# Kernel tuning notes

Hardware: AMD Instinct MI355X
Metric: run time of the kernel (lower is better)

## Reference

```python
import jax, jax.numpy as jnp
import numpy as np

# Dimensions
B, T = 128, 512
H = 256            # lstm_hiddens; encoder width is 2*H
LIN = 200          # linear_hiddens (LSTMCell input size)
PD, WD = 50, 20    # pos_dims, wordlen_dims
PN, WN = 32, 8     # pos_num, wordlen_num (word len clipped to 7)
SP = 58            # segpos_num
APP_ID = 0         # id of the APP action (forbidden at t=0)


def setup_inputs() -> dict:
    key = jax.random.key(0)
    ks = jax.random.split(key, 13)
    enc = jax.random.normal(ks[0], (B, T, 2 * H), dtype=jnp.float32)
    sep_mask = jax.random.randint(ks[1], (B, T), 0, 2, dtype=jnp.int32)
    sep_mask = sep_mask.at[:, 0].set(1)  # first action is always SEP (APP forbidden at t=0)
    pos_ids = jax.random.randint(ks[2], (B, T), 0, PN, dtype=jnp.int32)
    length = jax.random.randint(ks[3], (B,), T // 2, T + 1, dtype=jnp.int32)
    s = 0.05
    pos_emb = jax.random.normal(ks[4], (PN, PD), dtype=jnp.float32) * s
    wordlen_emb = jax.random.normal(ks[5], (WN, WD), dtype=jnp.float32) * s
    fc_W = jax.random.normal(ks[6], (LIN, PD + 2 * H + WD), dtype=jnp.float32) * s
    fc_b = jax.random.normal(ks[7], (LIN,), dtype=jnp.float32) * s
    W_ih = jax.random.normal(ks[8], (4 * H, LIN), dtype=jnp.float32) * s
    W_hh = jax.random.normal(ks[9], (4 * H, H), dtype=jnp.float32) * s
    b_ih = jax.random.normal(ks[10], (4 * H,), dtype=jnp.float32) * s
    b_hh = jax.random.normal(ks[11], (4 * H,), dtype=jnp.float32) * s
    combine_W = jax.random.normal(ks[12], (SP, 3 * H), dtype=jnp.float32) * s
    return {"encoder_output": enc, "sep_mask": sep_mask, "pos_ids": pos_ids,
            "length": length, "pos_emb": pos_emb, "wordlen_emb": wordlen_emb,
            "fc_W": fc_W, "fc_b": fc_b, "W_ih": W_ih, "W_hh": W_hh,
            "b_ih": b_ih, "b_hh": b_hh, "combine_W": combine_W}


def reference(encoder_output, sep_mask, pos_ids, length, pos_emb, wordlen_emb,
              fc_W, fc_b, W_ih, W_hh, b_ih, b_hh, combine_W):
    b, t, h2 = encoder_output.shape
    h = h2 // 2
    idx = jnp.arange(t, dtype=jnp.int32)

    # last SEP position strictly before t (word start of the in-progress word)
    sep_pos = jnp.where(sep_mask > 0, idx[None, :], 0)            # [B,T]
    cmax = jax.lax.cummax(sep_pos, axis=1)                        # last sep <= t
    last_sep = jnp.concatenate(
        [jnp.zeros((b, 1), jnp.int32), cmax[:, :-1]], axis=1)     # last sep < t

    wlen = idx[None, :] - last_sep                                # [B,T]; >=1 for t>=1
    wlen_safe = jnp.maximum(wlen, 1)
    wlen_id = jnp.minimum(wlen_safe, 7)                           # clip: len>6 -> 7

    # mean of encoder states over the current word [last_sep, t) via cumsum
    csum = jnp.concatenate(
        [jnp.zeros((b, 1, h2), encoder_output.dtype),
         jnp.cumsum(encoder_output, axis=1)], axis=1)             # [B,T+1,2H]
    start_sum = jnp.take_along_axis(csum, last_sep[:, :, None], axis=1)
    word_avg = (csum[:, :t] - start_sum) / wlen_safe[:, :, None].astype(encoder_output.dtype)

    last_pos = jnp.take_along_axis(pos_ids, last_sep, axis=1)     # [B,T]
    feats = jnp.concatenate(
        [pos_emb[last_pos], word_avg, wordlen_emb[wlen_id]], axis=-1)  # [B,T,PD+2H+WD]
    z = jnp.tanh(jnp.einsum('btf,lf->btl', feats, fc_W) + fc_b)   # [B,T,LIN]
    z = z.at[:, 0].set(0.0)                                       # step 0 input is zeros

    # LSTMCell recurrence over time (torch gate order: i, f, g, o)
    def step(carry, zt):
        hh, cc = carry
        g = zt @ W_ih.T + b_ih + hh @ W_hh.T + b_hh               # [B,4H]
        i, f, gg, o = jnp.split(g, 4, axis=-1)
        cc = jax.nn.sigmoid(f) * cc + jax.nn.sigmoid(i) * jnp.tanh(gg)
        hh = jax.nn.sigmoid(o) * jnp.tanh(cc)
        return (hh, cc), hh

    h0 = jnp.zeros((b, h), encoder_output.dtype)
    _, hs = jax.lax.scan(step, (h0, h0), jnp.swapaxes(z, 0, 1))   # hs: [T,B,H]
    hs = jnp.swapaxes(hs, 0, 1)                                   # [B,T,H]

    v = jnp.concatenate([hs, encoder_output], axis=-1)            # [B,T,3H]
    logits = jnp.einsum('btv,sv->bts', v, combine_W)              # [B,T,SP]
    logits = logits.at[:, 0, APP_ID].set(-1e30)                   # forbid APP at t=0 (in-place, no grad)
    valid = (idx[None, :] < length[:, None])[:, :, None]
    logits = jnp.where(valid, logits, 0.0)                        # pad steps emit zeros
    return logits.reshape(b * t, SP)
```

## Files before the change

### kernel.cpp

```cpp
#include <hip/hip_runtime.h>

typedef unsigned short ushort_t;
typedef unsigned int uint32;
typedef __attribute__((ext_vector_type(8))) short short8;
typedef __attribute__((ext_vector_type(4))) short short4v;
typedef __attribute__((ext_vector_type(4))) float floatx4;
typedef __attribute__((ext_vector_type(2))) float float2v;
typedef __attribute__((ext_vector_type(8))) int intx8;

#define B_    128
#define T_    512
#define H_    256
#define H2_   512
#define LIN_  200
#define LINP_ 224
#define G4_   1024
#define SP_   58
#define BT_   (B_*T_)

#define OFF_LS     0UL
#define OFF_LP     262144UL
#define OFF_WID    524288UL
#define OFF_INV    786432UL
#define OFF_POSW   1212416UL
#define OFF_WLW    1238016UL
#define OFF_BIASG  1244416UL
#define OFF_WHH    1248512UL
#define OFF_WIH    1772800UL
#define OFF_WENC   2231552UL
#define OFF_COMBW  2436352UL
#define OFF_ECW    2525440UL
#define OFF_Z      28739840UL
#define OFF_GPERM  58099968UL
#define OFF_VBF    192317696UL

__device__ __forceinline__ ushort_t f2bf(float x){
  uint32 u = __float_as_uint(x);
  u += 0x7fffu + ((u >> 16) & 1u);
  return (ushort_t)(u >> 16);
}
__device__ __forceinline__ float bf2f(ushort_t v){
  return __uint_as_float(((uint32)v) << 16);
}
__device__ __forceinline__ float fsig(float x){
  return __builtin_amdgcn_rcpf(1.0f + __expf(-x));
}
__device__ __forceinline__ float ftanh(float x){
  return 1.0f - 2.0f * __builtin_amdgcn_rcpf(1.0f + __expf(2.0f * x));
}

__global__ __launch_bounds__(512) void k_scan(const int* __restrict__ sep, const int* __restrict__ pos_ids,
                       int* __restrict__ ls, int* __restrict__ lp,
                       int* __restrict__ wid, float* __restrict__ inv){
  int b = blockIdx.x, t = threadIdx.x;
  __shared__ int sm[512];
  int v = (sep[b*T_ + t] > 0) ? t : 0;
  sm[t] = v;
  __syncthreads();
  #pragma unroll
  for (int off = 1; off < 512; off <<= 1){
    int o = (t >= off) ? sm[t - off] : 0;
    __syncthreads();
    v = (o > v) ? o : v;
    sm[t] = v;
    __syncthreads();
  }
  int l = (t == 0) ? 0 : sm[t - 1];
  int wlen = t - l;
  int wsv  = (wlen < 1) ? 1 : wlen;
  ls[b*T_ + t]  = l;
  lp[b*T_ + t]  = pos_ids[b*T_ + l];
  wid[b*T_ + t] = (wsv > 7) ? 7 : wsv;
  inv[b*T_ + t] = 1.0f / (float)wsv;
}

__global__ __launch_bounds__(256) void k_encbf(const float* __restrict__ enc, ushort_t* __restrict__ vbf){
  const long total = (long)BT_ * 128;
  for (long i = (long)blockIdx.x * 256 + threadIdx.x; i < total; i += 2048L * 256){
    floatx4 v = ((const floatx4*)enc)[i];
    long row = i >> 7;
    int c4 = (int)(i & 127);
    int b = (int)(row >> 9), t = (int)(row & (T_-1));
    short4v pk;
    pk[0] = (short)f2bf(v[0]); pk[1] = (short)f2bf(v[1]);
    pk[2] = (short)f2bf(v[2]); pk[3] = (short)f2bf(v[3]);
    *(short4v*)(void*)(vbf + ((long)t * B_ + b) * 768 + 256 + c4*4) = pk;
  }
}

__global__ __launch_bounds__(256) void k_small(
    const float* __restrict__ pos_emb, const float* __restrict__ wl_emb,
    const float* __restrict__ fcW, const float* __restrict__ W_ih,
    const float* __restrict__ W_hh, const float* __restrict__ b_ih,
    const float* __restrict__ b_hh, const float* __restrict__ combW,
    float* __restrict__ posW, float* __restrict__ wlW, float* __restrict__ biasg,
    char* __restrict__ whh8, ushort_t* __restrict__ wih,
    ushort_t* __restrict__ wenc, ushort_t* __restrict__ combwb){
  int idx = blockIdx.x * 256 + threadIdx.x;
  if (idx < 6400){
    int p = idx / 200, l = idx % 200;
    float s = 0.f;
    for (int d = 0; d < 50; d++) s += pos_emb[p*50 + d] * fcW[l*582 + d];
    posW[idx] = s; return;
  }
  idx -= 6400;
  if (idx < 1600){
    int w = idx / 200, l = idx % 200;
    float s = 0.f;
    for (int d = 0; d < 20; d++) s += wl_emb[w*20 + d] * fcW[l*582 + 562 + d];
    wlW[idx] = s; return;
  }
  idx -= 1600;
  if (idx < 1024){ biasg[idx] = b_ih[idx] + b_hh[idx]; return; }
  idx -= 1024;
  if (idx < 262144){
    int p8 = __builtin_amdgcn_cvt_pk_fp8_f32(W_hh[idx], W_hh[idx], 0, false);
    whh8[idx] = (char)(p8 & 0xff);
    return;
  }
  idx -= 262144;
  if (idx < 229376){
    int n = idx / 224, k = idx % 224;
    wih[idx] = (k < 200) ? f2bf(W_ih[n*200 + k]) : (ushort_t)0;
    return;
  }
  idx -= 229376;
  if (idx < 102400){
    int l = idx / 512, c = idx % 512;
    wenc[idx] = f2bf(fcW[l*582 + 50 + c]); return;
  }
  idx -= 102400;
  if (idx < 44544){ combwb[idx] = f2bf(combW[idx]); return; }
}

template<int EPI>
__global__ __launch_bounds__(256) void k_gemm(
    const ushort_t* __restrict__ A, long lda,
    const ushort_t* __restrict__ Bm, int K, int Nvalid,
    void* __restrict__ Cout, const float* __restrict__ bias, const int* __restrict__ len){
  __shared__ __attribute__((aligned(16))) ushort_t As[64][48];
  __shared__ __attribute__((aligned(16))) ushort_t Bs[64][48];
  int tid  = threadIdx.x;
  int lane = tid & 63, wave = tid >> 6;
  int u = lane & 15, quad = lane >> 4;
  int mh = wave >> 1, nh = wave & 1;
  long m0 = (long)blockIdx.y * 64;
  int  n0 = blockIdx.x * 64;
  int lrow = tid >> 2;
  int lcol = (tid & 3) * 8;
  const ushort_t* Arow = A + (m0 + lrow) * lda + lcol;
  bool bvalid = (n0 + lrow) < Nvalid;
  const ushort_t* Brow = Bm + (long)(n0 + lrow) * K + lcol;
  floatx4 acc[2][2] = {};
  for (int k = 0; k < K; k += 32){
    short8 av = *(const short8*)(const void*)(Arow + k);
    short8 bv = {0,0,0,0,0,0,0,0};
    if (bvalid) bv = *(const short8*)(const void*)(Brow + k);
    __syncthreads();
    *(short8*)(void*)&As[lrow][lcol] = av;
    *(short8*)(void*)&Bs[lrow][lcol] = bv;
    __syncthreads();
    short8 a0 = *(const short8*)(const void*)&As[mh*32 + u][quad*8];
    short8 a1 = *(const short8*)(const void*)&As[mh*32 + 16 + u][quad*8];
    short8 b0 = *(const short8*)(const void*)&Bs[nh*32 + u][quad*8];
    short8 b1 = *(const short8*)(const void*)&Bs[nh*32 + 16 + u][quad*8];
    acc[0][0] = __builtin_amdgcn_mfma_f32_16x16x32_bf16(a0, b0, acc[0][0], 0, 0, 0);
    acc[0][1] = __builtin_amdgcn_mfma_f32_16x16x32_bf16(a0, b1, acc[0][1], 0, 0, 0);
    acc[1][0] = __builtin_amdgcn_mfma_f32_16x16x32_bf16(a1, b0, acc[1][0], 0, 0, 0);
    acc[1][1] = __builtin_amdgcn_mfma_f32_16x16x32_bf16(a1, b1, acc[1][1], 0, 0, 0);
  }
  if (EPI == 1){
    #pragma unroll
    for (int mi = 0; mi < 2; mi++){
      #pragma unroll
      for (int ni = 0; ni < 2; ni++){
        long mm = m0 + mh*32 + mi*16 + quad*4;
        int n = n0 + nh*32 + ni*16 + u;
        float bv = bias[n];
        int t = (int)(mm >> 7);
        int b = (int)(mm & 127);
        int blk = b >> 2;
        int g = n >> 8, j = n & 255, ut = j & 15, jt = j >> 4;
        long idx = ((((long)t*32 + blk)*16 + jt)*4 + g)*64 + ut*4;
        short4v pk;
        #pragma unroll
        for (int r = 0; r < 4; r++) pk[r] = (short)f2bf(acc[mi][ni][r] + bv);
        *(short4v*)(void*)((ushort_t*)Cout + idx) = pk;
      }
    }
  } else {
    for (int mi = 0; mi < 2; mi++){
      for (int ni = 0; ni < 2; ni++){
        for (int r = 0; r < 4; r++){
          long m = m0 + mh*32 + mi*16 + quad*4 + r;
          int  n = n0 + nh*32 + ni*16 + u;
          float v = acc[mi][ni][r];
          if (EPI == 0){
            if (n < Nvalid) ((ushort_t*)Cout)[m * Nvalid + n] = f2bf(v);
          } else {
            if (n < Nvalid){
              int t = (int)(m >> 7); int b = (int)(m & 127);
              float o = (t < len[b]) ? v : 0.0f;
              if (t == 0 && n == 0) o = -1e30f;
              ((float*)Cout)[((long)b * T_ + t) * SP_ + n] = o;
            }
          }
        }
      }
    }
  }
}

__global__ __launch_bounds__(256) void k_cum200(ushort_t* __restrict__ E){
  int b = blockIdx.x;
  int c = threadIdx.x;
  if (c >= LIN_) return;
  float acc = 0.f;
  ushort_t* p = E + (long)b * LIN_ + c;
  const long rs = (long)B_ * LIN_;
  for (int t0 = 0; t0 < T_; t0 += 16){
    float vv[16];
    #pragma unroll
    for (int i = 0; i < 16; i++) vv[i] = bf2f(p[i*rs]);
    #pragma unroll
    for (int i = 0; i < 16; i++){ p[i*rs] = f2bf(acc); acc += vv[i]; }
    p += 16*rs;
  }
}

__global__ __launch_bounds__(256) void k_z(
    const ushort_t* __restrict__ CW, const int* __restrict__ ls, const int* __restrict__ lp,
    const int* __restrict__ wid, const float* __restrict__ inv,
    const float* __restrict__ posW, const float* __restrict__ wlW,
    const float* __restrict__ fcb, ushort_t* __restrict__ zbf){
  int l = threadIdx.x;
  if (l >= LINP_) return;
  float fb = (l < LIN_) ? fcb[l] : 0.f;
  #pragma unroll
  for (int i = 0; i < 8; i++){
    int m = blockIdx.x * 8 + i;
    int t = m >> 7;
    int b = m & 127;
    int ar = b * T_ + t;
    ushort_t o = 0;
    if (t != 0 && l < LIN_){
      int lsv = ls[ar];
      float x = bf2f(CW[(long)m * LIN_ + l]) - bf2f(CW[((long)lsv * B_ + b) * LIN_ + l]);
      x = x * inv[ar] + posW[lp[ar]*LIN_ + l] + wlW[wid[ar]*LIN_ + l] + fb;
      o = f2bf(ftanh(x));
    }
    zbf[(long)m * LINP_ + l] = o;
  }
}

__global__ __launch_bounds__(1024, 4) void k_rec(
    const ushort_t* __restrict__ Gperm, const char* __restrict__ whh8,
    ushort_t* __restrict__ vbf){
  int blk  = blockIdx.x;
  int tid  = threadIdx.x;
  int lane = tid & 63, w = tid >> 6;
  int u = lane & 15, quad = lane >> 4;
  __shared__ __attribute__((aligned(16))) char h8[2][16][272];
  for (int i = tid; i < (int)(sizeof(h8)/4); i += 1024) ((int*)h8)[i] = 0;

  intx8 wfx[4][2];
  #pragma unroll
  for (int g = 0; g < 4; g++){
    int grow = g*256 + w*16 + u;
    #pragma unroll
    for (int kc = 0; kc < 2; kc++){
      intx8 v = *(const intx8*)(const void*)(whh8 + (long)grow*256 + kc*128 + quad*32);
      asm volatile("" : "+v"(v));
      wfx[g][kc] = v;
    }
  }
  float c_reg = 0.f;
  floatx4 acc[4] = {};

  const ushort_t* gp0 = Gperm + ((long)blk*16 + w)*256 + (long)u*4 + quad;
  ushort_t gb[4];
  #pragma unroll
  for (int g = 0; g < 4; g++) gb[g] = gp0[g*64];

  for (int t = 0; t < T_; t++){
    #pragma unroll
    for (int g = 0; g < 4; g++) acc[g][0] = bf2f(gb[g]);
    asm volatile("s_waitcnt lgkmcnt(0)\n\ts_barrier" ::: "memory");
    intx8 af0 = *(const intx8*)(const void*)&h8[t & 1][u][quad*32];
    intx8 af1 = *(const intx8*)(const void*)&h8[t & 1][u][128 + quad*32];
    if (t && w < 4){
      ushort_t* vrow = vbf + ((long)(t-1) * B_ + blk*4 + w) * 768;
      uint32 p = *(const uint32*)(const void*)&h8[t & 1][4*w][lane*4];
      float2v lo = __builtin_amdgcn_cvt_pk_f32_fp8(p, false);
      float2v hi = __builtin_amdgcn_cvt_pk_f32_fp8(p, true);
      short4v pk;
      pk[0] = (short)f2bf(lo[0]); pk[1] = (short)f2bf(lo[1]);
      pk[2] = (short)f2bf(hi[0]); pk[3] = (short)f2bf(hi[1]);
      *(short4v*)(void*)&vrow[lane*4] = pk;
    }
    if (t + 1 < T_){
      const ushort_t* gp = gp0 + (long)(t+1)*131072;
      #pragma unroll
      for (int g = 0; g < 4; g++) gb[g] = gp[g*64];
    }
    acc[0] = __builtin_amdgcn_mfma_scale_f32_16x16x128_f8f6f4(
        af0, wfx[0][0], acc[0], 0, 0, 0, 0x7F7F7F7F, 0, 0x7F7F7F7F);
    acc[0] = __builtin_amdgcn_mfma_scale_f32_16x16x128_f8f6f4(
        af1, wfx[0][1], acc[0], 0, 0, 0, 0x7F7F7F7F, 0, 0x7F7F7F7F);
    acc[1] = __builtin_amdgcn_mfma_scale_f32_16x16x128_f8f6f4(
        af0, wfx[1][0], acc[1], 0, 0, 0, 0x7F7F7F7F, 0, 0x7F7F7F7F);
    acc[1] = __builtin_amdgcn_mfma_scale_f32_16x16x128_f8f6f4(
        af1, wfx[1][1], acc[1], 0, 0, 0, 0x7F7F7F7F, 0, 0x7F7F7F7F);
    float iv = fsig (acc[0][0]);
    float fv = fsig (acc[1][0]);
    acc[2] = __builtin_amdgcn_mfma_scale_f32_16x16x128_f8f6f4(
        af0, wfx[2][0], acc[2], 0, 0, 0, 0x7F7F7F7F, 0, 0x7F7F7F7F);
    acc[2] = __builtin_amdgcn_mfma_scale_f32_16x16x128_f8f6f4(
        af1, wfx[2][1], acc[2], 0, 0, 0, 0x7F7F7F7F, 0, 0x7F7F7F7F);
    acc[3] = __builtin_amdgcn_mfma_scale_f32_16x16x128_f8f6f4(
        af0, wfx[3][0], acc[3], 0, 0, 0, 0x7F7F7F7F, 0, 0x7F7F7F7F);
    acc[3] = __builtin_amdgcn_mfma_scale_f32_16x16x128_f8f6f4(
        af1, wfx[3][1], acc[3], 0, 0, 0, 0x7F7F7F7F, 0, 0x7F7F7F7F);
    float gv = ftanh(acc[2][0]);
    float ov = fsig (acc[3][0]);
    float c  = fv * c_reg + iv * gv;
    c_reg = c;
    float h  = ov * ftanh(c);
    int p8 = __builtin_amdgcn_cvt_pk_fp8_f32(h, h, 0, false);
    h8[(t+1)&1][quad*4][w*16 + u] = (char)(p8 & 0xff);
  }
  __syncthreads();
  if (w < 4){
    ushort_t* vrow = vbf + ((long)(T_-1) * B_ + blk*4 + w) * 768;
    uint32 p = *(const uint32*)(const void*)&h8[0][4*w][lane*4];
    float2v lo = __builtin_amdgcn_cvt_pk_f32_fp8(p, false);
    float2v hi = __builtin_amdgcn_cvt_pk_f32_fp8(p, true);
    short4v pk;
    pk[0] = (short)f2bf(lo[0]); pk[1] = (short)f2bf(lo[1]);
    pk[2] = (short)f2bf(hi[0]); pk[3] = (short)f2bf(hi[1]);
    *(short4v*)(void*)&vrow[lane*4] = pk;
  }
}

extern "C" void kernel_launch(void* const* d_in, const int* in_sizes, int n_in,
                              void* d_out, int out_size, void* d_ws, size_t ws_size,
                              hipStream_t stream){
  (void)in_sizes; (void)n_in; (void)out_size; (void)ws_size;
  const float* enc     = (const float*)d_in[0];
  const int*   sep     = (const int*)  d_in[1];
  const int*   pos_ids = (const int*)  d_in[2];
  const int*   len     = (const int*)  d_in[3];
  const float* pos_emb = (const float*)d_in[4];
  const float* wl_emb  = (const float*)d_in[5];
  const float* fcW     = (const float*)d_in[6];
  const float* fcb     = (const float*)d_in[7];
  const float* W_ih    = (const float*)d_in[8];
  const float* W_hh    = (const float*)d_in[9];
  const float* b_ih    = (const float*)d_in[10];
  const float* b_hh    = (const float*)d_in[11];
  const float* combW   = (const float*)d_in[12];

  char* ws = (char*)d_ws;
  int*      ls    = (int*)     (ws + OFF_LS);
  int*      lp    = (int*)     (ws + OFF_LP);
  int*      wid   = (int*)     (ws + OFF_WID);
  float*    inv   = (float*)   (ws + OFF_INV);
  float*    posW  = (float*)   (ws + OFF_POSW);
  float*    wlW   = (float*)   (ws + OFF_WLW);
  float*    biasg = (float*)   (ws + OFF_BIASG);
  char*     whh8  = (char*)    (ws + OFF_WHH);
  ushort_t* wih   = (ushort_t*)(ws + OFF_WIH);
  ushort_t* wenc  = (ushort_t*)(ws + OFF_WENC);
  ushort_t* combwb= (ushort_t*)(ws + OFF_COMBW);
  ushort_t* ecw   = (ushort_t*)(ws + OFF_ECW);
  ushort_t* zbf   = (ushort_t*)(ws + OFF_Z);
  ushort_t* gperm = (ushort_t*)(ws + OFF_GPERM);
  ushort_t* vbf   = (ushort_t*)(ws + OFF_VBF);

  k_scan<<<B_, 512, 0, stream>>>(sep, pos_ids, ls, lp, wid, inv);
  k_encbf<<<2048, 256, 0, stream>>>(enc, vbf);
  k_small<<<2530, 256, 0, stream>>>(pos_emb, wl_emb, fcW, W_ih, W_hh, b_ih, b_hh, combW,
                                    posW, wlW, biasg, whh8, wih, wenc, combwb);
  k_gemm<0><<<dim3(4, BT_/64), 256, 0, stream>>>(vbf + 256, 768L, wenc, 512, LIN_, ecw, nullptr, nullptr);
  k_cum200<<<B_, 256, 0, stream>>>(ecw);
  k_z<<<BT_/8, 256, 0, stream>>>(ecw, ls, lp, wid, inv, posW, wlW, fcb, zbf);
  k_gemm<1><<<dim3(16, BT_/64), 256, 0, stream>>>(zbf, (long)LINP_, wih, LINP_, G4_, gperm, biasg, nullptr);
  k_rec<<<32, 1024, 0, stream>>>(gperm, whh8, vbf);
  k_gemm<2><<<dim3(1, BT_/64), 256, 0, stream>>>(vbf, 768L, combwb, 768, SP_, d_out, nullptr, len);
}
```

Before: 876.8 us.

## Replace input-gate GEMM with 128x128 tiled kernel using direct global-to-LDS loads

Adds a dedicated kernel for the z·W_ih GEMM that computes 128x128 output tiles, with each wave covering a 64x64 sub-tile, instead of 64x64 tiles per block. Operands are loaded with global_load_lds straight into shared memory, skipping the trip through registers. The aim is more operand reuse per LDS load and less global traffic for this large GEMM. The bias plus permuted bf16 epilogue is moved over unchanged. The generic GEMM loses its EPI==1 branch, and the LDS layout is unpadded, which risks bank conflicts.

New measurement: 871.8 us. About the same (-0.6%).

```diff
diff --git a/kernel.cpp b/kernel.cpp
--- a/kernel.cpp
+++ b/kernel.cpp
@@ -169,44 +169,88 @@
     acc[1][0] = __builtin_amdgcn_mfma_f32_16x16x32_bf16(a1, b0, acc[1][0], 0, 0, 0);
     acc[1][1] = __builtin_amdgcn_mfma_f32_16x16x32_bf16(a1, b1, acc[1][1], 0, 0, 0);
   }
-  if (EPI == 1){
-    #pragma unroll
-    for (int mi = 0; mi < 2; mi++){
-      #pragma unroll
-      for (int ni = 0; ni < 2; ni++){
-        long mm = m0 + mh*32 + mi*16 + quad*4;
-        int n = n0 + nh*32 + ni*16 + u;
-        float bv = bias[n];
-        int t = (int)(mm >> 7);
-        int b = (int)(mm & 127);
-        int blk = b >> 2;
-        int g = n >> 8, j = n & 255, ut = j & 15, jt = j >> 4;
-        long idx = ((((long)t*32 + blk)*16 + jt)*4 + g)*64 + ut*4;
-        short4v pk;
-        #pragma unroll
-        for (int r = 0; r < 4; r++) pk[r] = (short)f2bf(acc[mi][ni][r] + bv);
-        *(short4v*)(void*)((ushort_t*)Cout + idx) = pk;
-      }
-    }
-  } else {
-    for (int mi = 0; mi < 2; mi++){
-      for (int ni = 0; ni < 2; ni++){
-        for (int r = 0; r < 4; r++){
-          long m = m0 + mh*32 + mi*16 + quad*4 + r;
-          int  n = n0 + nh*32 + ni*16 + u;
-          float v = acc[mi][ni][r];
-          if (EPI == 0){
-            if (n < Nvalid) ((ushort_t*)Cout)[m * Nvalid + n] = f2bf(v);
-          } else {
-            if (n < Nvalid){
-              int t = (int)(m >> 7); int b = (int)(m & 127);
-              float o = (t < len[b]) ? v : 0.0f;
-              if (t == 0 && n == 0) o = -1e30f;
-              ((float*)Cout)[((long)b * T_ + t) * SP_ + n] = o;
-            }
+  for (int mi = 0; mi < 2; mi++){
+    for (int ni = 0; ni < 2; ni++){
+      for (int r = 0; r < 4; r++){
+        long m = m0 + mh*32 + mi*16 + quad*4 + r;
+        int  n = n0 + nh*32 + ni*16 + u;
+        float v = acc[mi][ni][r];
+        if (EPI == 0){
+          if (n < Nvalid) ((ushort_t*)Cout)[m * Nvalid + n] = f2bf(v);
+        } else {
+          if (n < Nvalid){
+            int t = (int)(m >> 7); int b = (int)(m & 127);
+            float o = (t < len[b]) ? v : 0.0f;
+            if (t == 0 && n == 0) o = -1e30f;
+            ((float*)Cout)[((long)b * T_ + t) * SP_ + n] = o;
           }
         }
       }
+    }
+  }
+}
+
+__global__ __launch_bounds__(256) void k_g128(
+    const ushort_t* __restrict__ A,
+    const ushort_t* __restrict__ Bm,
+    ushort_t* __restrict__ Cout, const float* __restrict__ bias){
+  __shared__ __attribute__((aligned(16))) ushort_t As[128][32];
+  __shared__ __attribute__((aligned(16))) ushort_t Bs[128][32];
+  int tid  = threadIdx.x;
+  int lane = tid & 63, w = tid >> 6;
+  int u = lane & 15, quad = lane >> 4;
+  int wm = w >> 1, wn = w & 1;
+  long m0 = (long)blockIdx.y * 128;
+  int  n0 = blockIdx.x * 128;
+  int srow = lane >> 2;
+  int scol = (lane & 3) * 8;
+  floatx4 acc[4][4] = {};
+  for (int k = 0; k < LINP_; k += 32){
+    __syncthreads();
+    #pragma unroll
+    for (int c = 0; c < 2; c++){
+      int ch = w + c*4;
+      const ushort_t* sa = A + (m0 + ch*16 + srow) * (long)LINP_ + k + scol;
+      __builtin_amdgcn_global_load_lds(
+          (const __attribute__((address_space(1))) void*)sa,
+          (__attribute__((address_space(3))) void*)((char*)&As[0][0] + ch*1024),
+          16, 0, 0);
+      const ushort_t* sb = Bm + (long)(n0 + ch*16 + srow) * LINP_ + k + scol;
+      __builtin_amdgcn_global_load_lds(
+          (const __attribute__((address_space(1))) void*)sb,
+          (__attribute__((address_space(3))) void*)((char*)&Bs[0][0] + ch*1024),
+          16, 0, 0);
+    }
+    __syncthreads();
+    short8 af[4], bfr[4];
+    #pragma unroll
+    for (int mi = 0; mi < 4; mi++)
+      af[mi] = *(const short8*)(const void*)&As[wm*64 + mi*16 + u][quad*8];
+    #pragma unroll
+    for (int ni = 0; ni < 4; ni++)
+      bfr[ni] = *(const short8*)(const void*)&Bs[wn*64 + ni*16 + u][quad*8];
+    #pragma unroll
+    for (int mi = 0; mi < 4; mi++)
+      #pragma unroll
+      for (int ni = 0; ni < 4; ni++)
+        acc[mi][ni] = __builtin_amdgcn_mfma_f32_16x16x32_bf16(af[mi], bfr[ni], acc[mi][ni], 0, 0, 0);
+  }
+  #pragma unroll
+  for (int mi = 0; mi < 4; mi++){
+    #pragma unroll
+    for (int ni = 0; ni < 4; ni++){
+      long mm = m0 + wm*64 + mi*16 + quad*4;
+      int n = n0 + wn*64 + ni*16 + u;
+      float bv = bias[n];
+      int t = (int)(mm >> 7);
+      int b = (int)(mm & 127);
+      int blk = b >> 2;
+      int g = n >> 8, j = n & 255, ut = j & 15, jt = j >> 4;
+      long idx = ((((long)t*32 + blk)*16 + jt)*4 + g)*64 + ut*4;
+      short4v pk;
+      #pragma unroll
+      for (int r = 0; r < 4; r++) pk[r] = (short)f2bf(acc[mi][ni][r] + bv);
+      *(short4v*)(void*)(Cout + idx) = pk;
     }
   }
 }
@@ -384,7 +428,7 @@
   k_gemm<0><<<dim3(4, BT_/64), 256, 0, stream>>>(vbf + 256, 768L, wenc, 512, LIN_, ecw, nullptr, nullptr);
   k_cum200<<<B_, 256, 0, stream>>>(ecw);
   k_z<<<BT_/8, 256, 0, stream>>>(ecw, ls, lp, wid, inv, posW, wlW, fcb, zbf);
-  k_gemm<1><<<dim3(16, BT_/64), 256, 0, stream>>>(zbf, (long)LINP_, wih, LINP_, G4_, gperm, biasg, nullptr);
+  k_g128<<<dim3(8, BT_/128), 256, 0, stream>>>(zbf, wih, gperm, biasg);
   k_rec<<<32, 1024, 0, stream>>>(gperm, whh8, vbf);
   k_gemm<2><<<dim3(1, BT_/64), 256, 0, stream>>>(vbf, 768L, combwb, 768, SP_, d_out, nullptr, len);
 }
```

## Add large-tile double-buffered MFMA GEMM with direct global-to-LDS loads

Applied to the files above, without the earlier changes.

Adds a new GEMM kernel with a 128x256 block tile and 512 threads, where each wave computes a 64x64 sub-tile using 4x4 MFMA accumulators. K-slices are staged into double-buffered, XOR-swizzled LDS through global_load_lds, so the next slice loads while the current one computes. The encoder projection GEMM and the input-gate GEMM now use this kernel instead of the small 64x64 tile kernel; the old kernel keeps only the generic epilogue for the logits. The aim is more data reuse per LDS load and fewer block launches, at the cost of higher register pressure. The N=200 case also reads weight rows past the valid range, relying on the workspace layout to keep that safe.

Measured after the change: 823.0 us. 6.1% less time.

```diff
diff --git a/kernel.cpp b/kernel.cpp
--- a/kernel.cpp
+++ b/kernel.cpp
@@ -169,13 +169,98 @@
     acc[1][0] = __builtin_amdgcn_mfma_f32_16x16x32_bf16(a1, b0, acc[1][0], 0, 0, 0);
     acc[1][1] = __builtin_amdgcn_mfma_f32_16x16x32_bf16(a1, b1, acc[1][1], 0, 0, 0);
   }
+  for (int mi = 0; mi < 2; mi++){
+    for (int ni = 0; ni < 2; ni++){
+      for (int r = 0; r < 4; r++){
+        long m = m0 + mh*32 + mi*16 + quad*4 + r;
+        int  n = n0 + nh*32 + ni*16 + u;
+        float v = acc[mi][ni][r];
+        if (EPI == 0){
+          if (n < Nvalid) ((ushort_t*)Cout)[m * Nvalid + n] = f2bf(v);
+        } else {
+          if (n < Nvalid){
+            int t = (int)(m >> 7); int b = (int)(m & 127);
+            float o = (t < len[b]) ? v : 0.0f;
+            if (t == 0 && n == 0) o = -1e30f;
+            ((float*)Cout)[((long)b * T_ + t) * SP_ + n] = o;
+          }
+        }
+      }
+    }
+  }
+}
+
+template<int EPI>
+__global__ __launch_bounds__(512, 2) void k_big(
+    const ushort_t* __restrict__ A, long lda,
+    const ushort_t* __restrict__ Bm, int K, int Nvalid,
+    void* __restrict__ Cout, const float* __restrict__ bias){
+  __shared__ __attribute__((aligned(16))) ushort_t As[2][128][32];
+  __shared__ __attribute__((aligned(16))) ushort_t Bs[2][256][32];
+  int tid  = threadIdx.x;
+  int lane = tid & 63, w = tid >> 6;
+  int u = lane & 15, quad = lane >> 4;
+  int wm = w >> 2, wn = w & 3;
+  long m0 = (long)blockIdx.y * 128;
+  int  n0 = blockIdx.x * 256;
+  int sr = lane >> 2;
+  int gp = lane & 3;
+  int gl = gp ^ ((sr >> 1) & 3);
+  int arow = w*16 + sr;
+  const ushort_t* asrc = A + (m0 + arow) * lda + gl*8;
+  int brow = w*32 + sr;
+  const ushort_t* bsrc0 = Bm + (long)(n0 + brow) * K + gl*8;
+  const ushort_t* bsrc1 = Bm + (long)(n0 + brow + 16) * K + gl*8;
+  floatx4 acc[4][4] = {};
+
+#define STAGEK(buf, kk) do{ \
+    __builtin_amdgcn_global_load_lds( \
+        (const __attribute__((address_space(1))) void*)(asrc + (kk)), \
+        (__attribute__((address_space(3))) void*)((char*)&As[buf][0][0] + w*1024), 16, 0, 0); \
+    __builtin_amdgcn_global_load_lds( \
+        (const __attribute__((address_space(1))) void*)(bsrc0 + (kk)), \
+        (__attribute__((address_space(3))) void*)((char*)&Bs[buf][0][0] + w*2048), 16, 0, 0); \
+    __builtin_amdgcn_global_load_lds( \
+        (const __attribute__((address_space(1))) void*)(bsrc1 + (kk)), \
+        (__attribute__((address_space(3))) void*)((char*)&Bs[buf][0][0] + w*2048 + 1024), 16, 0, 0); \
+  }while(0)
+
+  STAGEK(0, 0);
+  asm volatile("s_waitcnt vmcnt(0)\n\ts_barrier" ::: "memory");
+  int nk = K >> 5;
+  int cur = 0;
+  for (int ks = 0; ks < nk; ks++){
+    if (ks + 1 < nk) STAGEK(cur ^ 1, (ks + 1) << 5);
+    short8 af[4], bfv[4];
+    #pragma unroll
+    for (int mi = 0; mi < 4; mi++){
+      int row = wm*64 + mi*16 + u;
+      int off = (row*64 + quad*16) ^ (((row >> 1) & 3) << 4);
+      af[mi] = *(const short8*)(const void*)((const char*)&As[cur][0][0] + off);
+    }
+    #pragma unroll
+    for (int ni = 0; ni < 4; ni++){
+      int row = wn*64 + ni*16 + u;
+      int off = (row*64 + quad*16) ^ (((row >> 1) & 3) << 4);
+      bfv[ni] = *(const short8*)(const void*)((const char*)&Bs[cur][0][0] + off);
+    }
+    #pragma unroll
+    for (int mi = 0; mi < 4; mi++)
+      #pragma unroll
+      for (int ni = 0; ni < 4; ni++)
+        acc[mi][ni] = __builtin_amdgcn_mfma_f32_16x16x32_bf16(af[mi], bfv[ni], acc[mi][ni], 0, 0, 0);
+    asm volatile("s_waitcnt vmcnt(0)\n\ts_barrier" ::: "memory");
+    cur ^= 1;
+  }
+#undef STAGEK
+
   if (EPI == 1){
     #pragma unroll
-    for (int mi = 0; mi < 2; mi++){
+    for (int mi = 0; mi < 4; mi++){
       #pragma unroll
-      for (int ni = 0; ni < 2; ni++){
-        long mm = m0 + mh*32 + mi*16 + quad*4;
-        int n = n0 + nh*32 + ni*16 + u;
+      for (int ni = 0; ni < 4; ni++){
+        long mm = m0 + wm*64 + mi*16 + quad*4;
+        int n = n0 + wn*64 + ni*16 + u;
         float bv = bias[n];
         int t = (int)(mm >> 7);
         int b = (int)(mm & 127);
@@ -189,21 +274,14 @@
       }
     }
   } else {
-    for (int mi = 0; mi < 2; mi++){
-      for (int ni = 0; ni < 2; ni++){
-        for (int r = 0; r < 4; r++){
-          long m = m0 + mh*32 + mi*16 + quad*4 + r;
-          int  n = n0 + nh*32 + ni*16 + u;
-          float v = acc[mi][ni][r];
-          if (EPI == 0){
-            if (n < Nvalid) ((ushort_t*)Cout)[m * Nvalid + n] = f2bf(v);
-          } else {
-            if (n < Nvalid){
-              int t = (int)(m >> 7); int b = (int)(m & 127);
-              float o = (t < len[b]) ? v : 0.0f;
-              if (t == 0 && n == 0) o = -1e30f;
-              ((float*)Cout)[((long)b * T_ + t) * SP_ + n] = o;
-            }
+    for (int mi = 0; mi < 4; mi++){
+      for (int ni = 0; ni < 4; ni++){
+        int n = n0 + wn*64 + ni*16 + u;
+        if (n < Nvalid){
+          #pragma unroll
+          for (int r = 0; r < 4; r++){
+            long m = m0 + wm*64 + mi*16 + quad*4 + r;
+            ((ushort_t*)Cout)[m * Nvalid + n] = f2bf(acc[mi][ni][r]);
           }
         }
       }
@@ -381,10 +459,10 @@
   k_encbf<<<2048, 256, 0, stream>>>(enc, vbf);
   k_small<<<2530, 256, 0, stream>>>(pos_emb, wl_emb, fcW, W_ih, W_hh, b_ih, b_hh, combW,
                                     posW, wlW, biasg, whh8, wih, wenc, combwb);
-  k_gemm<0><<<dim3(4, BT_/64), 256, 0, stream>>>(vbf + 256, 768L, wenc, 512, LIN_, ecw, nullptr, nullptr);
+  k_big<0><<<dim3(1, BT_/128), 512, 0, stream>>>(vbf + 256, 768L, wenc, 512, LIN_, ecw, nullptr);
   k_cum200<<<B_, 256, 0, stream>>>(ecw);
   k_z<<<BT_/8, 256, 0, stream>>>(ecw, ls, lp, wid, inv, posW, wlW, fcb, zbf);
-  k_gemm<1><<<dim3(16, BT_/64), 256, 0, stream>>>(zbf, (long)LINP_, wih, LINP_, G4_, gperm, biasg, nullptr);
+  k_big<1><<<dim3(4, BT_/128), 512, 0, stream>>>(zbf, (long)LINP_, wih, LINP_, G4_, gperm, biasg);
   k_rec<<<32, 1024, 0, stream>>>(gperm, whh8, vbf);
-  k_gemm<2><<<dim3(1, BT_/64), 256, 0, stream>>>(vbf, 768L, combwb, 768, SP_, d_out, nullptr, len);
-}
+  k_gemm<1><<<dim3(1, BT_/64), 256, 0, stream>>>(vbf, 768L, combwb, 768, SP_, d_out, nullptr, len);
+}
```
